# Kernel optimization log

Hardware: AMD Instinct MI355X
Metric: run time of the kernel (lower is better)

The kernel has to match this reference:

```python
import jax, jax.numpy as jnp
import numpy as np

NUM_HEADS = 12
ROPE_BASE = 10000.0


def _rope_cache(u, v, head_dim):
    # u, v: [n, L] normalized coords; P pairs per axis = head_dim // 4
    P = head_dim // 2 // 2
    freqs = jnp.arange(P) / (P - 1 + 1e-09)
    inv = 1.0 / ROPE_BASE ** freqs
    ang_x = jnp.einsum('nl,f->nlf', u, inv)
    ang_y = jnp.einsum('nl,f->nlf', v, inv)
    return jnp.cos(ang_x), jnp.sin(ang_x), jnp.cos(ang_y), jnp.sin(ang_y)


def _rope_apply(t, cos_x, sin_x, cos_y, sin_y):
    # t: [n, L, H, D]
    n, L, H, D = t.shape
    q = t.reshape(n, L, H, D // 2, 2)
    ppa = (D // 2) // 2  # pairs per axis
    qx, qy = jnp.split(q, [ppa], axis=-2)

    def rotate(qp, c, s):
        c = c[:, :, None, :]
        s = s[:, :, None, :]
        x, y = qp[..., 0], qp[..., 1]
        return jnp.stack([x * c - y * s, x * s + y * c], axis=-1)

    qx = rotate(qx, cos_x, sin_x)
    qy = rotate(qy, cos_y, sin_y)
    return jnp.concatenate([qx, qy], axis=-2).reshape(n, L, H, D)


def setup_inputs() -> dict:
    key = jax.random.key(0)
    ks = jax.random.split(key, 10)
    n, L, d = 16, 1024, 768
    H = NUM_HEADS
    D = d // H
    glorot = jax.nn.initializers.xavier_uniform()
    return {
        'inputs_q': jax.random.normal(ks[0], (n, L, d), jnp.float32),
        'inputs_kv': jax.random.normal(ks[1], (n, L, d), jnp.float32),
        'Wq': glorot(ks[2], (d, H, D), jnp.float32),
        'bq': jnp.zeros((H, D), jnp.float32),
        'Wk': glorot(ks[3], (d, H, D), jnp.float32),
        'bk': jnp.zeros((H, D), jnp.float32),
        'Wv': glorot(ks[4], (d, H, D), jnp.float32),
        'bv': jnp.zeros((H, D), jnp.float32),
        'Wo': glorot(ks[5], (H, D, d), jnp.float32),
        'bo': jnp.zeros((d,), jnp.float32),
    }


def reference(inputs_q, inputs_kv, Wq, bq, Wk, bk, Wv, bv, Wo, bo):
    n, L, d = inputs_q.shape
    H = NUM_HEADS
    D = d // H

    q = jnp.einsum('nld,dhk->nlhk', inputs_q, Wq) + bq
    k = jnp.einsum('nld,dhk->nlhk', inputs_kv, Wk) + bk
    v = jnp.einsum('nld,dhk->nlhk', inputs_kv, Wv) + bv

    # square-grid 2D RoPE coordinates (rope_uv=None fallback)
    h = w = int(np.sqrt(L))
    ys, xs = np.mgrid[:h, :w]
    u = jnp.tile(((xs.reshape(-1) + 0.5) / w).astype(np.float32)[None, :], (n, 1))
    vv = jnp.tile(((ys.reshape(-1) + 0.5) / h).astype(np.float32)[None, :], (n, 1))
    cos_x, sin_x, cos_y, sin_y = _rope_cache(u, vv, D)

    q = _rope_apply(q, cos_x, sin_x, cos_y, sin_y)
    k = _rope_apply(k, cos_x, sin_x, cos_y, sin_y)

    scale = 1.0 / jnp.sqrt(jnp.float32(D))
    attn_logits = jnp.einsum('nqhd,nkhd->nhqk', q, k) * scale
    attn = jax.nn.softmax(attn_logits, axis=-1)
    out = jnp.einsum('nhqk,nkhd->nqhd', attn, v)
    return jnp.einsum('nqhd,hdm->nqm', out, Wo) + bo
```

## Files before the change

kernel.cpp:

```cpp
#include <hip/hip_runtime.h>
#include <cmath>

#define DMODEL 768
#define SEQ    1024
#define NH     12
#define HDIM   64
#define MTOT   16384

typedef unsigned short ushort_t;
typedef __attribute__((ext_vector_type(8))) short short8v;
typedef __attribute__((ext_vector_type(4))) float f32x4;
typedef __attribute__((ext_vector_type(16))) float f32x16;
typedef __attribute__((ext_vector_type(2))) int i32x2v;

union v8u { short8v v; unsigned u[4]; };

__device__ __forceinline__ ushort_t bf16rn(float x) {
  unsigned u = __float_as_uint(x);
  return (ushort_t)((u + 0x7FFFu + ((u >> 16) & 1u)) >> 16);
}
__device__ __forceinline__ void bsplit(float x, ushort_t& h, ushort_t& l) {
  h = bf16rn(x);
  float hf = __uint_as_float((unsigned)h << 16);
  l = bf16rn(x - hf);
}

__device__ __forceinline__ unsigned cvt_pk_bf16(float a, float b) {
  unsigned r;
  asm("v_cvt_pk_bf16_f32 %0, %1, %2" : "=v"(r) : "v"(a), "v"(b));
  return r;
}
__device__ __forceinline__ void bsplit2(float x0, float x1, unsigned& hw, unsigned& lw) {
  hw = cvt_pk_bf16(x0, x1);
  const float h0 = __uint_as_float(hw << 16);
  const float h1 = __uint_as_float(hw & 0xFFFF0000u);
  lw = cvt_pk_bf16(x0 - h0, x1 - h1);
}

__device__ __forceinline__ float vmax3(float a, float b, float c) {
  float d;
  asm("v_max3_f32 %0, %1, %2, %3" : "=v"(d) : "v"(a), "v"(b), "v"(c));
  return d;
}

__device__ __forceinline__ i32x2v pl32(unsigned a, unsigned b) {
  return __builtin_amdgcn_permlane32_swap((int)a, (int)b, false, false);
}

__device__ __forceinline__ void gld16(const void* g, void* l) {
  __builtin_amdgcn_global_load_lds(
      (const __attribute__((address_space(1))) int*)g,
      (__attribute__((address_space(3))) int*)l, 16, 0, 0);
}

__global__ __launch_bounds__(256)
void rope_table_kernel(float* __restrict__ tab) {
  int idx = blockIdx.x * 256 + threadIdx.x;
  if (idx >= SEQ * 16) return;
  int l = idx >> 4, p = idx & 15;
  double u = ((double)(l & 31) + 0.5) / 32.0;
  double v = ((double)(l >> 5) + 0.5) / 32.0;
  double freq = (double)p / (15.0 + 1e-9);
  double inv = pow(10000.0, -freq);
  tab[idx]         = (float)cos(u * inv);
  tab[16384 + idx] = (float)sin(u * inv);
  tab[32768 + idx] = (float)cos(v * inv);
  tab[49152 + idx] = (float)sin(v * inv);
}

__global__ __launch_bounds__(256)
void split_x_kernel(const float* __restrict__ X, ushort_t* __restrict__ H,
                    ushort_t* __restrict__ L) {
  const int i = blockIdx.x * 256 + threadIdx.x;
  const float4 a = ((const float4*)X)[i * 2];
  const float4 b = ((const float4*)X)[i * 2 + 1];
  v8u h, l;
  bsplit2(a.x, a.y, h.u[0], l.u[0]);
  bsplit2(a.z, a.w, h.u[1], l.u[1]);
  bsplit2(b.x, b.y, h.u[2], l.u[2]);
  bsplit2(b.z, b.w, h.u[3], l.u[3]);
  ((short8v*)H)[i] = h.v;
  ((short8v*)L)[i] = l.v;
}

__global__ __launch_bounds__(256)
void wsplit_t_kernel(const float* __restrict__ W, ushort_t* __restrict__ TH,
                     ushort_t* __restrict__ TL) {
  __shared__ __align__(16) float T[64][65];
  const int t = threadIdx.x;
  const int kt = blockIdx.x, nt = blockIdx.y;
  const int r = t >> 2, c4 = (t & 3) * 16;
  const float* src = W + (size_t)(kt * 64 + r) * DMODEL + nt * 64 + c4;
#pragma unroll
  for (int i = 0; i < 16; i += 4)
    *(float4*)&T[r][c4 + i] = *(const float4*)&src[i];
  __syncthreads();
  short8v h0, h1, l0, l1;
#pragma unroll
  for (int i = 0; i < 8; ++i) {
    ushort_t hh, ll;
    bsplit(T[c4 + i][r], hh, ll);
    h0[i] = (short)hh; l0[i] = (short)ll;
  }
#pragma unroll
  for (int i = 0; i < 8; ++i) {
    ushort_t hh, ll;
    bsplit(T[c4 + 8 + i][r], hh, ll);
    h1[i] = (short)hh; l1[i] = (short)ll;
  }
  const size_t o = (size_t)(nt * 64 + r) * DMODEL + kt * 64 + c4;
  *(short8v*)&TH[o] = h0; *(short8v*)&TH[o + 8] = h1;
  *(short8v*)&TL[o] = l0; *(short8v*)&TL[o + 8] = l1;
}

__global__ __launch_bounds__(256)
void gemm_mfma_kernel(const ushort_t* __restrict__ Ahi, const ushort_t* __restrict__ Alo,
                      const ushort_t* __restrict__ Bhi, const ushort_t* __restrict__ Blo,
                      const float* __restrict__ bias, float* __restrict__ Cout,
                      ushort_t* __restrict__ Ohi, ushort_t* __restrict__ Olo,
                      const float* __restrict__ rope, int mode, float oscale) {
  __shared__ __align__(16) ushort_t Ah[128][32];
  __shared__ __align__(16) ushort_t Al[128][32];
  __shared__ __align__(16) ushort_t Bh[128][32];
  __shared__ __align__(16) ushort_t Bl[128][32];

  const int t = threadIdx.x, lane = t & 63, w = t >> 6;
  const int l15 = lane & 15, l4 = lane >> 4;
  const int wm = w >> 1, wn = w & 1;
  const int m0 = blockIdx.y * 128, n0 = blockIdx.x * 128;

  const int crow = t >> 2, ccc = (t & 3) * 8;
  const ushort_t* pAh0 = Ahi + (size_t)(m0 + crow) * DMODEL + ccc;
  const ushort_t* pAh1 = pAh0 + (size_t)64 * DMODEL;
  const ushort_t* pAl0 = Alo + (size_t)(m0 + crow) * DMODEL + ccc;
  const ushort_t* pAl1 = pAl0 + (size_t)64 * DMODEL;
  const ushort_t* pBh0 = Bhi + (size_t)(n0 + crow) * DMODEL + ccc;
  const ushort_t* pBh1 = pBh0 + (size_t)64 * DMODEL;
  const ushort_t* pBl0 = Blo + (size_t)(n0 + crow) * DMODEL + ccc;
  const ushort_t* pBl1 = pBl0 + (size_t)64 * DMODEL;
  void* dAh0 = &Ah[crow][ccc];      void* dAh1 = &Ah[crow + 64][ccc];
  void* dAl0 = &Al[crow][ccc];      void* dAl1 = &Al[crow + 64][ccc];
  void* dBh0 = &Bh[crow][ccc];      void* dBh1 = &Bh[crow + 64][ccc];
  void* dBl0 = &Bl[crow][ccc];      void* dBl1 = &Bl[crow + 64][ccc];

  f32x4 acc[4][4] = {};

  for (int ks = 0; ks < DMODEL / 32; ++ks) {
    __syncthreads();
    gld16(pAh0, dAh0); gld16(pAh1, dAh1);
    gld16(pAl0, dAl0); gld16(pAl1, dAl1);
    gld16(pBh0, dBh0); gld16(pBh1, dBh1);
    gld16(pBl0, dBl0); gld16(pBl1, dBl1);
    pAh0 += 32; pAh1 += 32; pAl0 += 32; pAl1 += 32;
    pBh0 += 32; pBh1 += 32; pBl0 += 32; pBl1 += 32;
    __syncthreads();

    short8v afh[4], afl[4], bfh[4], bfl[4];
#pragma unroll
    for (int f = 0; f < 4; ++f) {
      afh[f] = *(const short8v*)&Ah[wm * 64 + f * 16 + l15][l4 * 8];
      afl[f] = *(const short8v*)&Al[wm * 64 + f * 16 + l15][l4 * 8];
      bfh[f] = *(const short8v*)&Bh[wn * 64 + f * 16 + l15][l4 * 8];
      bfl[f] = *(const short8v*)&Bl[wn * 64 + f * 16 + l15][l4 * 8];
    }
#pragma unroll
    for (int mf = 0; mf < 4; ++mf)
#pragma unroll
      for (int nf = 0; nf < 4; ++nf) {
        acc[mf][nf] = __builtin_amdgcn_mfma_f32_16x16x32_bf16(afh[mf], bfh[nf], acc[mf][nf], 0, 0, 0);
        acc[mf][nf] = __builtin_amdgcn_mfma_f32_16x16x32_bf16(afl[mf], bfh[nf], acc[mf][nf], 0, 0, 0);
        acc[mf][nf] = __builtin_amdgcn_mfma_f32_16x16x32_bf16(afh[mf], bfl[nf], acc[mf][nf], 0, 0, 0);
      }
  }

  float bcol[4];
#pragma unroll
  for (int nf = 0; nf < 4; ++nf) bcol[nf] = bias[n0 + wn * 64 + nf * 16 + l15];

  if (mode == 0) {
#pragma unroll
    for (int mf = 0; mf < 4; ++mf)
#pragma unroll
      for (int r = 0; r < 4; ++r) {
        const int m = m0 + wm * 64 + mf * 16 + l4 * 4 + r;
#pragma unroll
        for (int nf = 0; nf < 4; ++nf)
          Cout[(size_t)m * DMODEL + n0 + wn * 64 + nf * 16 + l15] = acc[mf][nf][r] + bcol[nf];
      }
  } else {
    const int h = blockIdx.x * 2 + wn;
#pragma unroll
    for (int mf = 0; mf < 4; ++mf)
#pragma unroll
      for (int r = 0; r < 4; ++r) {
        const int m = m0 + wm * 64 + mf * 16 + l4 * 4 + r;
        const int l = m & (SEQ - 1);
        const int nb = m >> 10;
        const size_t orow = ((size_t)(nb * NH + h) * SEQ + l) * HDIM;
        float vv[4];
#pragma unroll
        for (int nf = 0; nf < 4; ++nf) {
          float v = acc[mf][nf][r] + bcol[nf];
          if (mode == 1) {
            const float vp = __shfl_xor(v, 1, 64);
            const int tb = (nf < 2) ? 0 : 32768;
            const int pi = (nf & 1) * 8 + (l15 >> 1);
            const float c = rope[tb + l * 16 + pi];
            const float s = rope[tb + 16384 + l * 16 + pi];
            v = (l15 & 1) ? (vp * s + v * c) : (v * c - vp * s);
            v *= oscale;
          }
          vv[nf] = v;
        }
        unsigned h01, l01, h23, l23;
        bsplit2(vv[0], vv[1], h01, l01);
        bsplit2(vv[2], vv[3], h23, l23);
        Ohi[orow + 0 * 16 + l15] = (ushort_t)(h01 & 0xFFFFu);
        Ohi[orow + 1 * 16 + l15] = (ushort_t)(h01 >> 16);
        Ohi[orow + 2 * 16 + l15] = (ushort_t)(h23 & 0xFFFFu);
        Ohi[orow + 3 * 16 + l15] = (ushort_t)(h23 >> 16);
        Olo[orow + 0 * 16 + l15] = (ushort_t)(l01 & 0xFFFFu);
        Olo[orow + 1 * 16 + l15] = (ushort_t)(l01 >> 16);
        Olo[orow + 2 * 16 + l15] = (ushort_t)(l23 & 0xFFFFu);
        Olo[orow + 3 * 16 + l15] = (ushort_t)(l23 >> 16);
      }
  }
}

__global__ __launch_bounds__(256)
void vtrans_kernel(const ushort_t* __restrict__ VH, const ushort_t* __restrict__ VL,
                   ushort_t* __restrict__ TH, ushort_t* __restrict__ TL) {
  __shared__ __align__(16) ushort_t Th[64][72];
  __shared__ __align__(16) ushort_t Tl[64][72];
  const int t = threadIdx.x;
  const int lt = blockIdx.x, h = blockIdx.y, n = blockIdx.z;
  const int r = t >> 2, c = (t & 3) * 16;
  const size_t src = ((size_t)(n * NH + h) * SEQ + lt * 64 + r) * HDIM + c;
  *(short8v*)&Th[r][c]     = *(const short8v*)&VH[src];
  *(short8v*)&Th[r][c + 8] = *(const short8v*)&VH[src + 8];
  *(short8v*)&Tl[r][c]     = *(const short8v*)&VL[src];
  *(short8v*)&Tl[r][c + 8] = *(const short8v*)&VL[src + 8];
  __syncthreads();
  short8v h0, h1, l0, l1;
#pragma unroll
  for (int i = 0; i < 8; ++i) { h0[i] = (short)Th[c + i][r];     l0[i] = (short)Tl[c + i][r]; }
#pragma unroll
  for (int i = 0; i < 8; ++i) { h1[i] = (short)Th[c + 8 + i][r]; l1[i] = (short)Tl[c + 8 + i][r]; }
  const size_t dst = ((size_t)(n * NH + h) * HDIM + r) * SEQ + lt * 64 + c;
  *(short8v*)&TH[dst]     = h0; *(short8v*)&TH[dst + 8] = h1;
  *(short8v*)&TL[dst]     = l0; *(short8v*)&TL[dst + 8] = l1;
}

__global__ __launch_bounds__(256)
void attn_mfma_kernel(const ushort_t* __restrict__ qh, const ushort_t* __restrict__ ql,
                      const ushort_t* __restrict__ kh, const ushort_t* __restrict__ kl,
                      const ushort_t* __restrict__ vth, const ushort_t* __restrict__ vtl,
                      ushort_t* __restrict__ abh, ushort_t* __restrict__ abl) {
  __shared__ __align__(16) ushort_t KHs[2][64][64];
  __shared__ __align__(16) ushort_t KLs[2][64][64];
  __shared__ __align__(16) ushort_t VHs[2][64][64];
  __shared__ __align__(16) ushort_t VLs[2][64][64];

  const int t = threadIdx.x;
  const int lane = t & 63, w = t >> 6;
  const int l31 = lane & 31, l1 = lane >> 5;

  const int bid = blockIdx.x;
  const int xcd = bid & 7, rest = bid >> 3;
  const int qt = rest & 7;
  const int hl = (rest >> 3) * 8 + xcd;
  const int h = hl % NH, n = hl / NH;

  const size_t base = (size_t)(n * NH + h) * (SEQ * HDIM);

  short8v qfh[4], qfl[4];
  {
    const size_t qoff = base + (size_t)(qt * 128 + w * 32 + l31) * HDIM + l1 * 8;
#pragma unroll
    for (int ks = 0; ks < 4; ++ks) {
      qfh[ks] = *(const short8v*)&qh[qoff + ks * 16];
      qfl[ks] = *(const short8v*)&ql[qoff + ks * 16];
    }
  }

  const int srow = lane >> 3;
  const int schk = (lane & 7) ^ srow;
  const int sA = 2 * w, sB = 2 * w + 1;
  const size_t kofA = base + (size_t)(sA * 8 + srow) * HDIM + schk * 8;
  const size_t kofB = base + (size_t)(sB * 8 + srow) * HDIM + schk * 8;
  const size_t vofA = base + (size_t)(sA * 8 + srow) * SEQ + schk * 8;
  const size_t vofB = base + (size_t)(sB * 8 + srow) * SEQ + schk * 8;
  const int drA = sA * 8 + srow, drB = sB * 8 + srow, dc = (lane & 7) * 8;

  f32x16 Oa0 = {}, Oa1 = {};
  f32x16 lpv = {};
  float mrun = 0.0f;

#define ATTN_ISSUE(kt_, b_) do {                                            \
    const size_t ko_ = (size_t)(kt_) * (64 * HDIM);                         \
    const size_t vo_ = (size_t)(kt_) * 64;                                  \
    gld16(kh  + kofA + ko_, &KHs[b_][drA][dc]);                             \
    gld16(kh  + kofB + ko_, &KHs[b_][drB][dc]);                             \
    gld16(kl  + kofA + ko_, &KLs[b_][drA][dc]);                             \
    gld16(kl  + kofB + ko_, &KLs[b_][drB][dc]);                             \
    gld16(vth + vofA + vo_, &VHs[b_][drA][dc]);                             \
    gld16(vth + vofB + vo_, &VHs[b_][drB][dc]);                             \
    gld16(vtl + vofA + vo_, &VLs[b_][drA][dc]);                             \
    gld16(vtl + vofB + vo_, &VLs[b_][drB][dc]);                             \
  } while (0)

  ATTN_ISSUE(0, 0);

  for (int kt = 0; kt < 16; ++kt) {
    const int cur = kt & 1;
    __syncthreads();
    if (kt < 15) ATTN_ISSUE(kt + 1, cur ^ 1);

    f32x16 S0 = {}, S1 = {};
    __builtin_amdgcn_s_setprio(1);
#pragma unroll
    for (int ks = 0; ks < 4; ++ks) {
      const int cc = ((2 * ks + l1) ^ (l31 & 7)) * 8;
      const short8v k0h = *(const short8v*)&KHs[cur][l31][cc];
      const short8v k0l = *(const short8v*)&KLs[cur][l31][cc];
      const short8v k1h = *(const short8v*)&KHs[cur][32 + l31][cc];
      const short8v k1l = *(const short8v*)&KLs[cur][32 + l31][cc];
      S0 = __builtin_amdgcn_mfma_f32_32x32x16_bf16(k0h, qfh[ks], S0, 0, 0, 0);
      S1 = __builtin_amdgcn_mfma_f32_32x32x16_bf16(k1h, qfh[ks], S1, 0, 0, 0);
      S0 = __builtin_amdgcn_mfma_f32_32x32x16_bf16(k0l, qfh[ks], S0, 0, 0, 0);
      S1 = __builtin_amdgcn_mfma_f32_32x32x16_bf16(k1l, qfh[ks], S1, 0, 0, 0);
      S0 = __builtin_amdgcn_mfma_f32_32x32x16_bf16(k0h, qfl[ks], S0, 0, 0, 0);
      S1 = __builtin_amdgcn_mfma_f32_32x32x16_bf16(k1h, qfl[ks], S1, 0, 0, 0);
    }
    __builtin_amdgcn_s_setprio(0);

    const float a0 = vmax3(S0[0],  S0[1],  S0[2]);
    const float a1 = vmax3(S0[3],  S0[4],  S0[5]);
    const float a2 = vmax3(S0[6],  S0[7],  S0[8]);
    const float a3 = vmax3(S0[9],  S0[10], S0[11]);
    const float a4 = vmax3(S0[12], S0[13], S0[14]);
    const float b0 = vmax3(S1[0],  S1[1],  S1[2]);
    const float b1 = vmax3(S1[3],  S1[4],  S1[5]);
    const float b2 = vmax3(S1[6],  S1[7],  S1[8]);
    const float b3 = vmax3(S1[9],  S1[10], S1[11]);
    const float b4 = vmax3(S1[12], S1[13], S1[14]);
    const float c0 = vmax3(a0, a1, a2);
    const float c1 = vmax3(a3, a4, S0[15]);
    const float c2 = vmax3(b0, b1, b2);
    const float c3 = vmax3(b3, b4, S1[15]);
    const float mx = fmaxf(vmax3(c0, c1, c2), c3);

    if (__all((mrun == 0.0f) & (mx <= 30.0f))) {
#pragma unroll
      for (int i = 0; i < 16; ++i) {
        S0[i] = __builtin_amdgcn_exp2f(S0[i]);
        S1[i] = __builtin_amdgcn_exp2f(S1[i]);
      }
      lpv += S0 + S1;
    } else {
      const float om = fmaxf(mx, __shfl_xor(mx, 32));
      const float nm = fmaxf(mrun, om);
      const float scl = __builtin_amdgcn_exp2f(mrun - nm);
      mrun = nm;
#pragma unroll
      for (int i = 0; i < 16; ++i) {
        S0[i] = __builtin_amdgcn_exp2f(S0[i] - nm);
        S1[i] = __builtin_amdgcn_exp2f(S1[i] - nm);
      }
      lpv = lpv * scl + (S0 + S1);
      Oa0 = Oa0 * scl;
      Oa1 = Oa1 * scl;
    }

#pragma unroll
    for (int half = 0; half < 2; ++half) {
      unsigned hx[4], hy[4], lx[4], ly[4];
#pragma unroll
      for (int m = 0; m < 4; ++m) {
        float p0, p1, p2, p3;
        if (half == 0) { p0 = S0[4*m]; p1 = S0[4*m+1]; p2 = S0[4*m+2]; p3 = S0[4*m+3]; }
        else           { p0 = S1[4*m]; p1 = S1[4*m+1]; p2 = S1[4*m+2]; p3 = S1[4*m+3]; }
        bsplit2(p0, p1, hx[m], lx[m]);
        bsplit2(p2, p3, hy[m], ly[m]);
      }
      __builtin_amdgcn_s_setprio(1);
#pragma unroll
      for (int kss = 0; kss < 2; ++kss) {
        const i32x2v rhx = pl32(hx[2*kss], hx[2*kss+1]);
        const i32x2v rhy = pl32(hy[2*kss], hy[2*kss+1]);
        const i32x2v rlx = pl32(lx[2*kss], lx[2*kss+1]);
        const i32x2v rly = pl32(ly[2*kss], ly[2*kss+1]);
        v8u bfh, bfl;
        bfh.u[0] = (unsigned)rhx[0]; bfh.u[1] = (unsigned)rhy[0];
        bfh.u[2] = (unsigned)rhx[1]; bfh.u[3] = (unsigned)rhy[1];
        bfl.u[0] = (unsigned)rlx[0]; bfl.u[1] = (unsigned)rly[0];
        bfl.u[2] = (unsigned)rlx[1]; bfl.u[3] = (unsigned)rly[1];
        const int cc = ((4*half + 2*kss + l1) ^ (l31 & 7)) * 8;
        const short8v v0h = *(const short8v*)&VHs[cur][l31][cc];
        const short8v v0l = *(const short8v*)&VLs[cur][l31][cc];
        const short8v v1h = *(const short8v*)&VHs[cur][32 + l31][cc];
        const short8v v1l = *(const short8v*)&VLs[cur][32 + l31][cc];
        Oa0 = __builtin_amdgcn_mfma_f32_32x32x16_bf16(v0h, bfh.v, Oa0, 0, 0, 0);
        Oa1 = __builtin_amdgcn_mfma_f32_32x32x16_bf16(v1h, bfh.v, Oa1, 0, 0, 0);
        Oa0 = __builtin_amdgcn_mfma_f32_32x32x16_bf16(v0l, bfh.v, Oa0, 0, 0, 0);
        Oa1 = __builtin_amdgcn_mfma_f32_32x32x16_bf16(v1l, bfh.v, Oa1, 0, 0, 0);
        Oa0 = __builtin_amdgcn_mfma_f32_32x32x16_bf16(v0h, bfl.v, Oa0, 0, 0, 0);
        Oa1 = __builtin_amdgcn_mfma_f32_32x32x16_bf16(v1h, bfl.v, Oa1, 0, 0, 0);
      }
      __builtin_amdgcn_s_setprio(0);
    }
  }

  float lp = ((((lpv[0]+lpv[1])+(lpv[2]+lpv[3]))+((lpv[4]+lpv[5])+(lpv[6]+lpv[7])))
           + (((lpv[8]+lpv[9])+(lpv[10]+lpv[11]))+((lpv[12]+lpv[13])+(lpv[14]+lpv[15]))));
  lp += __shfl_xor(lp, 32);
  const float inv = 1.0f / lp;
  const size_t orow = ((size_t)n * SEQ + qt * 128 + w * 32 + l31) * DMODEL + h * HDIM;
#pragma unroll
  for (int jd = 0; jd < 2; ++jd) {
#pragma unroll
    for (int g = 0; g < 4; ++g) {
      float o0, o1, o2, o3;
      if (jd == 0) { o0 = Oa0[4*g]; o1 = Oa0[4*g+1]; o2 = Oa0[4*g+2]; o3 = Oa0[4*g+3]; }
      else         { o0 = Oa1[4*g]; o1 = Oa1[4*g+1]; o2 = Oa1[4*g+2]; o3 = Oa1[4*g+3]; }
      o0 *= inv; o1 *= inv; o2 *= inv; o3 *= inv;
      unsigned h01, l01, h23, l23;
      bsplit2(o0, o1, h01, l01);
      bsplit2(o2, o3, h23, l23);
      const int d = 32 * jd + 8 * g + 4 * l1;
      uint2 sh; sh.x = h01; sh.y = h23;
      uint2 sl; sl.x = l01; sl.y = l23;
      *(uint2*)&abh[orow + d] = sh;
      *(uint2*)&abl[orow + d] = sl;
    }
  }
#undef ATTN_ISSUE
}

extern "C" void kernel_launch(void* const* d_in, const int* in_sizes, int n_in,
                              void* d_out, int out_size, void* d_ws, size_t ws_size,
                              hipStream_t stream) {
  (void)in_sizes; (void)n_in; (void)out_size;
  const float* Xq  = (const float*)d_in[0];
  const float* Xkv = (const float*)d_in[1];
  const float* Wq  = (const float*)d_in[2];
  const float* bq  = (const float*)d_in[3];
  const float* Wk  = (const float*)d_in[4];
  const float* bk  = (const float*)d_in[5];
  const float* Wv  = (const float*)d_in[6];
  const float* bv  = (const float*)d_in[7];
  const float* Wo  = (const float*)d_in[8];
  const float* bo  = (const float*)d_in[9];
  float* out = (float*)d_out;

  if (ws_size < 201588736ull) return;
  char* W = (char*)d_ws;
  const size_t HB = 25165824ull;
  float*    rope = (float*)W;
  ushort_t* xh  = (ushort_t*)(W + 262144);
  ushort_t* xl  = (ushort_t*)(W + 262144 + HB);
  ushort_t* vth = xh;
  ushort_t* vtl = xl;
  char* C0 = W + 262144 + 2 * HB;
  ushort_t* qhi = (ushort_t*)(C0);
  ushort_t* qlo = (ushort_t*)(C0 + HB);
  ushort_t* khi = (ushort_t*)(C0 + 2 * HB);
  ushort_t* klo = (ushort_t*)(C0 + 3 * HB);
  ushort_t* woth = (ushort_t*)(C0);
  ushort_t* wotl = woth + 589824;
  char* D0 = C0 + 4 * HB;
  ushort_t* vbh = (ushort_t*)(D0);
  ushort_t* vbl = (ushort_t*)(D0 + HB);
  ushort_t* abh = vbh;
  ushort_t* abl = vbl;
  ushort_t* wqth = (ushort_t*)d_out;            ushort_t* wqtl = wqth + 589824;
  ushort_t* wkth = wqth + 1179648;              ushort_t* wktl = wkth + 589824;
  ushort_t* wvth = wqth + 2359296;              ushort_t* wvtl = wvth + 589824;

  rope_table_kernel<<<64, 256, 0, stream>>>(rope);
  wsplit_t_kernel<<<dim3(12, 12), 256, 0, stream>>>(Wq, wqth, wqtl);
  wsplit_t_kernel<<<dim3(12, 12), 256, 0, stream>>>(Wk, wkth, wktl);
  wsplit_t_kernel<<<dim3(12, 12), 256, 0, stream>>>(Wv, wvth, wvtl);

  const dim3 gg(DMODEL / 128, MTOT / 128);
  const float q_scale = 0.125f * 1.44269504088896340736f;

  split_x_kernel<<<6144, 256, 0, stream>>>(Xq, xh, xl);
  gemm_mfma_kernel<<<gg, 256, 0, stream>>>(xh, xl, wqth, wqtl, bq, nullptr, qhi, qlo, rope, 1, q_scale);

  split_x_kernel<<<6144, 256, 0, stream>>>(Xkv, xh, xl);
  gemm_mfma_kernel<<<gg, 256, 0, stream>>>(xh, xl, wkth, wktl, bk, nullptr, khi, klo, rope, 1, 1.0f);
  gemm_mfma_kernel<<<gg, 256, 0, stream>>>(xh, xl, wvth, wvtl, bv, nullptr, vbh, vbl, rope, 2, 1.0f);

  vtrans_kernel<<<dim3(16, NH, 16), 256, 0, stream>>>(vbh, vbl, vth, vtl);

  attn_mfma_kernel<<<1536, 256, 0, stream>>>(qhi, qlo, khi, klo, vth, vtl, abh, abl);

  wsplit_t_kernel<<<dim3(12, 12), 256, 0, stream>>>(Wo, woth, wotl);
  gemm_mfma_kernel<<<gg, 256, 0, stream>>>(abh, abl, woth, wotl, bo, out, nullptr, nullptr, rope, 0, 1.0f);
}
```

Baseline: 580.9 us.

## Fuse fp32 input split into projection GEMMs and stage V loads separately in attention

```diff
diff --git a/kernel.cpp b/kernel.cpp
--- a/kernel.cpp
+++ b/kernel.cpp
@@ -69,21 +69,6 @@
 }
 
 __global__ __launch_bounds__(256)
-void split_x_kernel(const float* __restrict__ X, ushort_t* __restrict__ H,
-                    ushort_t* __restrict__ L) {
-  const int i = blockIdx.x * 256 + threadIdx.x;
-  const float4 a = ((const float4*)X)[i * 2];
-  const float4 b = ((const float4*)X)[i * 2 + 1];
-  v8u h, l;
-  bsplit2(a.x, a.y, h.u[0], l.u[0]);
-  bsplit2(a.z, a.w, h.u[1], l.u[1]);
-  bsplit2(b.x, b.y, h.u[2], l.u[2]);
-  bsplit2(b.z, b.w, h.u[3], l.u[3]);
-  ((short8v*)H)[i] = h.v;
-  ((short8v*)L)[i] = l.v;
-}
-
-__global__ __launch_bounds__(256)
 void wsplit_t_kernel(const float* __restrict__ W, ushort_t* __restrict__ TH,
                      ushort_t* __restrict__ TL) {
   __shared__ __align__(16) float T[64][65];
@@ -113,16 +98,20 @@
   *(short8v*)&TL[o] = l0; *(short8v*)&TL[o + 8] = l1;
 }
 
+template<int AFP32>
 __global__ __launch_bounds__(256)
-void gemm_mfma_kernel(const ushort_t* __restrict__ Ahi, const ushort_t* __restrict__ Alo,
+void gemm_mfma_kernel(const float* __restrict__ Af,
+                      const ushort_t* __restrict__ Ahi, const ushort_t* __restrict__ Alo,
                       const ushort_t* __restrict__ Bhi, const ushort_t* __restrict__ Blo,
                       const float* __restrict__ bias, float* __restrict__ Cout,
                       ushort_t* __restrict__ Ohi, ushort_t* __restrict__ Olo,
                       const float* __restrict__ rope, int mode, float oscale) {
-  __shared__ __align__(16) ushort_t Ah[128][32];
-  __shared__ __align__(16) ushort_t Al[128][32];
+  __shared__ __align__(16) unsigned char Araw[16384];
   __shared__ __align__(16) ushort_t Bh[128][32];
   __shared__ __align__(16) ushort_t Bl[128][32];
+  ushort_t (*Ah)[32] = (ushort_t(*)[32])Araw;
+  ushort_t (*Al)[32] = (ushort_t(*)[32])(Araw + 8192);
+  float* Afs = (float*)Araw;
 
   const int t = threadIdx.x, lane = t & 63, w = t >> 6;
   const int l15 = lane & 15, l4 = lane >> 4;
@@ -130,36 +119,66 @@
   const int m0 = blockIdx.y * 128, n0 = blockIdx.x * 128;
 
   const int crow = t >> 2, ccc = (t & 3) * 8;
-  const ushort_t* pAh0 = Ahi + (size_t)(m0 + crow) * DMODEL + ccc;
-  const ushort_t* pAh1 = pAh0 + (size_t)64 * DMODEL;
-  const ushort_t* pAl0 = Alo + (size_t)(m0 + crow) * DMODEL + ccc;
-  const ushort_t* pAl1 = pAl0 + (size_t)64 * DMODEL;
   const ushort_t* pBh0 = Bhi + (size_t)(n0 + crow) * DMODEL + ccc;
   const ushort_t* pBh1 = pBh0 + (size_t)64 * DMODEL;
   const ushort_t* pBl0 = Blo + (size_t)(n0 + crow) * DMODEL + ccc;
   const ushort_t* pBl1 = pBl0 + (size_t)64 * DMODEL;
-  void* dAh0 = &Ah[crow][ccc];      void* dAh1 = &Ah[crow + 64][ccc];
-  void* dAl0 = &Al[crow][ccc];      void* dAl1 = &Al[crow + 64][ccc];
   void* dBh0 = &Bh[crow][ccc];      void* dBh1 = &Bh[crow + 64][ccc];
   void* dBl0 = &Bl[crow][ccc];      void* dBl1 = &Bl[crow + 64][ccc];
 
+  const int sr8 = lane >> 3, sc8 = lane & 7, sg = sc8 ^ sr8;
+  const ushort_t* pAh0 = nullptr; const ushort_t* pAh1 = nullptr;
+  const ushort_t* pAl0 = nullptr; const ushort_t* pAl1 = nullptr;
+  void* dAh0 = nullptr; void* dAh1 = nullptr; void* dAl0 = nullptr; void* dAl1 = nullptr;
+  if (!AFP32) {
+    pAh0 = Ahi + (size_t)(m0 + crow) * DMODEL + ccc;
+    pAh1 = pAh0 + (size_t)64 * DMODEL;
+    pAl0 = Alo + (size_t)(m0 + crow) * DMODEL + ccc;
+    pAl1 = pAl0 + (size_t)64 * DMODEL;
+    dAh0 = &Ah[crow][ccc];  dAh1 = &Ah[crow + 64][ccc];
+    dAl0 = &Al[crow][ccc];  dAl1 = &Al[crow + 64][ccc];
+  }
+
   f32x4 acc[4][4] = {};
 
   for (int ks = 0; ks < DMODEL / 32; ++ks) {
     __syncthreads();
-    gld16(pAh0, dAh0); gld16(pAh1, dAh1);
-    gld16(pAl0, dAl0); gld16(pAl1, dAl1);
+    if (AFP32) {
+#pragma unroll
+      for (int j = 0; j < 4; ++j) {
+        const int row = j * 32 + w * 8 + sr8;
+        gld16(Af + (size_t)(m0 + row) * DMODEL + ks * 32 + sg * 4,
+              &Afs[row * 32 + sc8 * 4]);
+      }
+    } else {
+      gld16(pAh0, dAh0); gld16(pAh1, dAh1);
+      gld16(pAl0, dAl0); gld16(pAl1, dAl1);
+      pAh0 += 32; pAh1 += 32; pAl0 += 32; pAl1 += 32;
+    }
     gld16(pBh0, dBh0); gld16(pBh1, dBh1);
     gld16(pBl0, dBl0); gld16(pBl1, dBl1);
-    pAh0 += 32; pAh1 += 32; pAl0 += 32; pAl1 += 32;
     pBh0 += 32; pBh1 += 32; pBl0 += 32; pBl1 += 32;
     __syncthreads();
 
     short8v afh[4], afl[4], bfh[4], bfl[4];
 #pragma unroll
     for (int f = 0; f < 4; ++f) {
-      afh[f] = *(const short8v*)&Ah[wm * 64 + f * 16 + l15][l4 * 8];
-      afl[f] = *(const short8v*)&Al[wm * 64 + f * 16 + l15][l4 * 8];
+      if (AFP32) {
+        const int row = wm * 64 + f * 16 + l15;
+        const int rs = l15 & 7;
+        const float* ap = Afs + row * 32;
+        const f32x4 x0 = *(const f32x4*)(ap + (((2 * l4)     ^ rs) * 4));
+        const f32x4 x1 = *(const f32x4*)(ap + (((2 * l4 + 1) ^ rs) * 4));
+        v8u hh, ll;
+        bsplit2(x0[0], x0[1], hh.u[0], ll.u[0]);
+        bsplit2(x0[2], x0[3], hh.u[1], ll.u[1]);
+        bsplit2(x1[0], x1[1], hh.u[2], ll.u[2]);
+        bsplit2(x1[2], x1[3], hh.u[3], ll.u[3]);
+        afh[f] = hh.v; afl[f] = ll.v;
+      } else {
+        afh[f] = *(const short8v*)&Ah[wm * 64 + f * 16 + l15][l4 * 8];
+        afl[f] = *(const short8v*)&Al[wm * 64 + f * 16 + l15][l4 * 8];
+      }
       bfh[f] = *(const short8v*)&Bh[wn * 64 + f * 16 + l15][l4 * 8];
       bfl[f] = *(const short8v*)&Bl[wn * 64 + f * 16 + l15][l4 * 8];
     }
@@ -258,8 +277,8 @@
                       ushort_t* __restrict__ abh, ushort_t* __restrict__ abl) {
   __shared__ __align__(16) ushort_t KHs[2][64][64];
   __shared__ __align__(16) ushort_t KLs[2][64][64];
-  __shared__ __align__(16) ushort_t VHs[2][64][64];
-  __shared__ __align__(16) ushort_t VLs[2][64][64];
+  __shared__ __align__(16) ushort_t VHs[64][64];
+  __shared__ __align__(16) ushort_t VLs[64][64];
 
   const int t = threadIdx.x;
   const int lane = t & 63, w = t >> 6;
@@ -296,25 +315,28 @@
   f32x16 lpv = {};
   float mrun = 0.0f;
 
-#define ATTN_ISSUE(kt_, b_) do {                                            \
+#define ISSUE_V(kt_) do {                                                   \
+    const size_t vo_ = (size_t)(kt_) * 64;                                  \
+    gld16(vth + vofA + vo_, &VHs[drA][dc]);                                 \
+    gld16(vth + vofB + vo_, &VHs[drB][dc]);                                 \
+    gld16(vtl + vofA + vo_, &VLs[drA][dc]);                                 \
+    gld16(vtl + vofB + vo_, &VLs[drB][dc]);                                 \
+  } while (0)
+#define ISSUE_K(kt_, b_) do {                                               \
     const size_t ko_ = (size_t)(kt_) * (64 * HDIM);                         \
-    const size_t vo_ = (size_t)(kt_) * 64;                                  \
-    gld16(kh  + kofA + ko_, &KHs[b_][drA][dc]);                             \
-    gld16(kh  + kofB + ko_, &KHs[b_][drB][dc]);                             \
-    gld16(kl  + kofA + ko_, &KLs[b_][drA][dc]);                             \
-    gld16(kl  + kofB + ko_, &KLs[b_][drB][dc]);                             \
-    gld16(vth + vofA + vo_, &VHs[b_][drA][dc]);                             \
-    gld16(vth + vofB + vo_, &VHs[b_][drB][dc]);                             \
-    gld16(vtl + vofA + vo_, &VLs[b_][drA][dc]);                             \
-    gld16(vtl + vofB + vo_, &VLs[b_][drB][dc]);                             \
+    gld16(kh + kofA + ko_, &KHs[b_][drA][dc]);                              \
+    gld16(kh + kofB + ko_, &KHs[b_][drB][dc]);                              \
+    gld16(kl + kofA + ko_, &KLs[b_][drA][dc]);                              \
+    gld16(kl + kofB + ko_, &KLs[b_][drB][dc]);                              \
   } while (0)
 
-  ATTN_ISSUE(0, 0);
+  ISSUE_K(0, 0);
 
   for (int kt = 0; kt < 16; ++kt) {
     const int cur = kt & 1;
     __syncthreads();
-    if (kt < 15) ATTN_ISSUE(kt + 1, cur ^ 1);
+    ISSUE_V(kt);
+    if (kt < 15) ISSUE_K(kt + 1, cur ^ 1);
 
     f32x16 S0 = {}, S1 = {};
     __builtin_amdgcn_s_setprio(1);
@@ -372,6 +394,10 @@
       Oa1 = Oa1 * scl;
     }
 
+    if (kt < 15) { asm volatile("s_waitcnt vmcnt(4)" ::: "memory"); }
+    else         { asm volatile("s_waitcnt vmcnt(0)" ::: "memory"); }
+    __builtin_amdgcn_sched_barrier(0);
+
 #pragma unroll
     for (int half = 0; half < 2; ++half) {
       unsigned hx[4], hy[4], lx[4], ly[4];
@@ -396,10 +422,10 @@
         bfl.u[0] = (unsigned)rlx[0]; bfl.u[1] = (unsigned)rly[0];
         bfl.u[2] = (unsigned)rlx[1]; bfl.u[3] = (unsigned)rly[1];
         const int cc = ((4*half + 2*kss + l1) ^ (l31 & 7)) * 8;
-        const short8v v0h = *(const short8v*)&VHs[cur][l31][cc];
-        const short8v v0l = *(const short8v*)&VLs[cur][l31][cc];
-        const short8v v1h = *(const short8v*)&VHs[cur][32 + l31][cc];
-        const short8v v1l = *(const short8v*)&VLs[cur][32 + l31][cc];
+        const short8v v0h = *(const short8v*)&VHs[l31][cc];
+        const short8v v0l = *(const short8v*)&VLs[l31][cc];
+        const short8v v1h = *(const short8v*)&VHs[32 + l31][cc];
+        const short8v v1l = *(const short8v*)&VLs[32 + l31][cc];
         Oa0 = __builtin_amdgcn_mfma_f32_32x32x16_bf16(v0h, bfh.v, Oa0, 0, 0, 0);
         Oa1 = __builtin_amdgcn_mfma_f32_32x32x16_bf16(v1h, bfh.v, Oa1, 0, 0, 0);
         Oa0 = __builtin_amdgcn_mfma_f32_32x32x16_bf16(v0l, bfh.v, Oa0, 0, 0, 0);
@@ -434,7 +460,8 @@
       *(uint2*)&abl[orow + d] = sl;
     }
   }
-#undef ATTN_ISSUE
+#undef ISSUE_V
+#undef ISSUE_K
 }
 
 extern "C" void kernel_launch(void* const* d_in, const int* in_sizes, int n_in,
@@ -457,10 +484,8 @@
   char* W = (char*)d_ws;
   const size_t HB = 25165824ull;
   float*    rope = (float*)W;
-  ushort_t* xh  = (ushort_t*)(W + 262144);
-  ushort_t* xl  = (ushort_t*)(W + 262144 + HB);
-  ushort_t* vth = xh;
-  ushort_t* vtl = xl;
+  ushort_t* vth = (ushort_t*)(W + 262144);
+  ushort_t* vtl = (ushort_t*)(W + 262144 + HB);
   char* C0 = W + 262144 + 2 * HB;
   ushort_t* qhi = (ushort_t*)(C0);
   ushort_t* qlo = (ushort_t*)(C0 + HB);
@@ -485,17 +510,18 @@
   const dim3 gg(DMODEL / 128, MTOT / 128);
   const float q_scale = 0.125f * 1.44269504088896340736f;
 
-  split_x_kernel<<<6144, 256, 0, stream>>>(Xq, xh, xl);
-  gemm_mfma_kernel<<<gg, 256, 0, stream>>>(xh, xl, wqth, wqtl, bq, nullptr, qhi, qlo, rope, 1, q_scale);
-
-  split_x_kernel<<<6144, 256, 0, stream>>>(Xkv, xh, xl);
-  gemm_mfma_kernel<<<gg, 256, 0, stream>>>(xh, xl, wkth, wktl, bk, nullptr, khi, klo, rope, 1, 1.0f);
-  gemm_mfma_kernel<<<gg, 256, 0, stream>>>(xh, xl, wvth, wvtl, bv, nullptr, vbh, vbl, rope, 2, 1.0f);
+  gemm_mfma_kernel<1><<<gg, 256, 0, stream>>>(Xq, nullptr, nullptr, wqth, wqtl,
+                                              bq, nullptr, qhi, qlo, rope, 1, q_scale);
+  gemm_mfma_kernel<1><<<gg, 256, 0, stream>>>(Xkv, nullptr, nullptr, wkth, wktl,
+                                              bk, nullptr, khi, klo, rope, 1, 1.0f);
+  gemm_mfma_kernel<1><<<gg, 256, 0, stream>>>(Xkv, nullptr, nullptr, wvth, wvtl,
+                                              bv, nullptr, vbh, vbl, rope, 2, 1.0f);
 
   vtrans_kernel<<<dim3(16, NH, 16), 256, 0, stream>>>(vbh, vbl, vth, vtl);
 
   attn_mfma_kernel<<<1536, 256, 0, stream>>>(qhi, qlo, khi, klo, vth, vtl, abh, abl);
 
   wsplit_t_kernel<<<dim3(12, 12), 256, 0, stream>>>(Wo, woth, wotl);
-  gemm_mfma_kernel<<<gg, 256, 0, stream>>>(abh, abl, woth, wotl, bo, out, nullptr, nullptr, rope, 0, 1.0f);
-}
+  gemm_mfma_kernel<0><<<gg, 256, 0, stream>>>(nullptr, abh, abl, woth, wotl,
+                                              bo, out, nullptr, nullptr, rope, 0, 1.0f);
+}
```

After: 638.6 us. +9.9%, slower.
